# Kernel tuning notes

Hardware: AMD Instinct MI355X
Metric: run time of the kernel (lower is better)

The kernel has to match this reference:

```python
import jax, jax.numpy as jnp
import numpy as np

B, T, S, D, H, DK = 2, 2048, 2048, 1024, 16, 64


def setup_inputs() -> dict:
    key = jax.random.key(0)
    ks = jax.random.split(key, 11)
    s = 1.0 / np.sqrt(D)
    return {
        "query": jax.random.normal(ks[0], (B, T, D), jnp.float32),
        "value": jax.random.normal(ks[1], (B, S, D), jnp.float32),
        "key": jax.random.normal(ks[2], (B, S, D), jnp.float32),
        "Wq": jax.random.normal(ks[3], (D, H, DK), jnp.float32) * s,
        "bq": jnp.zeros((H, DK), jnp.float32),
        "Wk": jax.random.normal(ks[4], (D, H, DK), jnp.float32) * s,
        "bk": jnp.zeros((H, DK), jnp.float32),
        "Wv": jax.random.normal(ks[5], (D, H, DK), jnp.float32) * s,
        "bv": jnp.zeros((H, DK), jnp.float32),
        "Wo": jax.random.normal(ks[6], (H, DK, D), jnp.float32) * (1.0 / np.sqrt(H * DK)),
        "bo": jnp.zeros((D,), jnp.float32),
    }


def reference(query, value, key, Wq, bq, Wk, bk, Wv, bv, Wo, bo):
    # Projections: (B, seq, D) x (D, H, DK) -> (B, seq, H, DK)
    q = jnp.einsum("btd,dhk->bthk", query, Wq) + bq
    k = jnp.einsum("bsd,dhk->bshk", key, Wk) + bk
    v = jnp.einsum("bsd,dhk->bshk", value, Wv) + bv
    # Scaled dot-product attention (keras scales query by 1/sqrt(key_dim))
    q = q * (1.0 / np.sqrt(DK)).astype(np.float32)
    scores = jnp.einsum("bshk,bthk->bhts", k, q)  # (B, H, T, S)
    probs = jax.nn.softmax(scores, axis=-1)
    attn = jnp.einsum("bhts,bshk->bthk", probs, v)  # (B, T, H, DK)
    # Output projection back to model dim
    out = jnp.einsum("bthk,hkd->btd", attn, Wo) + bo
    return out
```

## Files before the change

### kernel.cpp

```cpp
#include <hip/hip_runtime.h>
#include <math.h>

#define BB  2
#define TT  2048
#define SSQ 2048
#define DD  1024
#define HH  16
#define DKK 64
#define MM  (BB*TT)
#define NN  (HH*DKK)

typedef __attribute__((ext_vector_type(8))) short short8;
typedef __attribute__((ext_vector_type(4))) float f32x4;
typedef __attribute__((ext_vector_type(2))) unsigned int u32x2;

__device__ __forceinline__ short f2bf(float x) {
    unsigned u = __builtin_bit_cast(unsigned, x);
    unsigned r = (u + 0x7FFFu + ((u >> 16) & 1u)) >> 16;
    return (short)r;
}

__device__ __forceinline__ void glds16(const void* g, void* l) {
    __builtin_amdgcn_global_load_lds(
        (const __attribute__((address_space(1))) void*)g,
        (__attribute__((address_space(3))) void*)l, 16, 0, 0);
}

__global__ __launch_bounds__(256)
void to_bf16_acts(const float* __restrict__ a0, const float* __restrict__ a1,
                  const float* __restrict__ a2,
                  short* __restrict__ o0, short* __restrict__ o1,
                  short* __restrict__ o2)
{
    int z = blockIdx.y;
    const float* in = (z == 0) ? a0 : (z == 1) ? a1 : a2;
    short* out = (z == 0) ? o0 : (z == 1) ? o1 : o2;
    size_t i0 = ((size_t)blockIdx.x * 256 + threadIdx.x) * 8;
    f32x4 f0 = *(const f32x4*)(in + i0);
    f32x4 f1 = *(const f32x4*)(in + i0 + 4);
    short8 v;
#pragma unroll
    for (int j = 0; j < 4; j++) v[j] = f2bf(f0[j]);
#pragma unroll
    for (int j = 0; j < 4; j++) v[4 + j] = f2bf(f1[j]);
    *(short8*)(out + i0) = v;
}

__global__ __launch_bounds__(256)
void wtrans(const float* __restrict__ w0, const float* __restrict__ w1,
            const float* __restrict__ w2, const float* __restrict__ w3,
            short* __restrict__ t0, short* __restrict__ t1,
            short* __restrict__ t2, short* __restrict__ t3)
{
    __shared__ float Ls[64][65];
    int z = blockIdx.z;
    const float* in = (z == 0) ? w0 : (z == 1) ? w1 : (z == 2) ? w2 : w3;
    short* out = (z == 0) ? t0 : (z == 1) ? t1 : (z == 2) ? t2 : t3;
    const int r0 = blockIdx.y * 64, c0 = blockIdx.x * 64;
    const int t = threadIdx.x;
    const int r = t >> 2, c4 = t & 3;

    const float* src = in + (size_t)(r0 + r) * DD + c0 + c4 * 16;
#pragma unroll
    for (int i = 0; i < 4; i++) {
        f32x4 f = *(const f32x4*)(src + i * 4);
#pragma unroll
        for (int j = 0; j < 4; j++) Ls[r][c4 * 16 + i * 4 + j] = f[j];
    }
    __syncthreads();

    short8 va, vb;
#pragma unroll
    for (int j = 0; j < 8; j++) va[j] = f2bf(Ls[c4 * 16 + j][r]);
#pragma unroll
    for (int j = 0; j < 8; j++) vb[j] = f2bf(Ls[c4 * 16 + 8 + j][r]);
    short* dst = out + (size_t)(c0 + r) * DD + r0 + c4 * 16;
    *(short8*)dst = va;
    *(short8*)(dst + 8) = vb;
}

__global__ __launch_bounds__(256)
void vtrans(const short* __restrict__ in, short* __restrict__ out)
{
    __shared__ short Ls[64][72];
    const int bh = blockIdx.y;
    const int t0 = blockIdx.x * 64;
    const int tid = threadIdx.x;
    const int r = tid >> 2, c4 = tid & 3;

    const short* src = in + ((size_t)bh * TT + t0 + r) * DKK + c4 * 16;
    *(short8*)&Ls[r][c4 * 16]     = *(const short8*)(src);
    *(short8*)&Ls[r][c4 * 16 + 8] = *(const short8*)(src + 8);
    __syncthreads();

    short8 a, b;
#pragma unroll
    for (int j = 0; j < 8; j++) a[j] = Ls[c4 * 16 + j][r];
#pragma unroll
    for (int j = 0; j < 8; j++) b[j] = Ls[c4 * 16 + 8 + j][r];
    short* dst = out + ((size_t)bh * DKK + r) * SSQ + t0 + c4 * 16;
    *(short8*)dst = a;
    *(short8*)(dst + 8) = b;
}

__device__ __forceinline__ void gemm_core(const short* __restrict__ A,
                                          const short* __restrict__ Bt,
                                          int m0, int n0,
                                          short* As, short* Bs,
                                          f32x4 (&acc)[4][4])
{
    const int tid = threadIdx.x;
    const int w = tid >> 6, l = tid & 63;
    const int l15 = l & 15, quad = l >> 4;
    const int wm = w >> 1, wn = w & 1;

#pragma unroll
    for (int i = 0; i < 4; i++)
#pragma unroll
        for (int j = 0; j < 4; j++) acc[i][j] = (f32x4){0.f, 0.f, 0.f, 0.f};

    const int r = tid >> 2, cseg = tid & 3;
    const short* gA = A + (size_t)(m0 + r) * DD + cseg * 8;
    const short* gB = Bt + (size_t)(n0 + r) * DD + cseg * 8;
    short* ldsA = As + w * 512;
    short* ldsB = Bs + w * 512;

    for (int k0 = 0; k0 < DD; k0 += 32) {
        glds16(gA + k0,                 ldsA);
        glds16(gA + (size_t)64 * DD + k0, ldsA + 2048);
        glds16(gB + k0,                 ldsB);
        glds16(gB + (size_t)64 * DD + k0, ldsB + 2048);
        __syncthreads();

        short8 bF[4];
#pragma unroll
        for (int ni = 0; ni < 4; ni++)
            bF[ni] = *(const short8*)&Bs[(wn * 64 + ni * 16 + l15) * 32 + quad * 8];
#pragma unroll
        for (int mi = 0; mi < 4; mi++) {
            short8 aF = *(const short8*)&As[(wm * 64 + mi * 16 + l15) * 32 + quad * 8];
#pragma unroll
            for (int ni = 0; ni < 4; ni++)
                acc[mi][ni] = __builtin_amdgcn_mfma_f32_16x16x32_bf16(aF, bF[ni], acc[mi][ni], 0, 0, 0);
        }
        __syncthreads();
    }
}

__global__ __launch_bounds__(256, 3)
void gemm_qkv(const short* __restrict__ Aq, const short* __restrict__ Ak,
              const short* __restrict__ Av,
              const short* __restrict__ Wqt, const short* __restrict__ Wkt,
              const short* __restrict__ Wvt,
              const float* __restrict__ bq, const float* __restrict__ bk,
              const float* __restrict__ bv,
              short* __restrict__ Qb, short* __restrict__ Kb,
              short* __restrict__ Vtmp)
{
    __shared__ short As[128 * 32];
    __shared__ short Bs[128 * 32];
    const int z = blockIdx.z;
    const short* A  = (z == 0) ? Aq : (z == 1) ? Ak : Av;
    const short* Bt = (z == 0) ? Wqt : (z == 1) ? Wkt : Wvt;
    const float* bias = (z == 0) ? bq : (z == 1) ? bk : bv;
    short* dst = (z == 0) ? Qb : (z == 1) ? Kb : Vtmp;
    const int m0 = blockIdx.y * 128, n0 = blockIdx.x * 128;

    f32x4 acc[4][4];
    gemm_core(A, Bt, m0, n0, As, Bs, acc);

    const int tid = threadIdx.x;
    const int w = tid >> 6, l = tid & 63;
    const int l15 = l & 15, quad = l >> 4;
    const int wm = w >> 1, wn = w & 1;
    const float scale = (z == 0) ? 0.1803368801f : 1.0f;

#pragma unroll
    for (int mi = 0; mi < 4; mi++) {
#pragma unroll
        for (int reg = 0; reg < 4; reg++) {
            int m = m0 + wm * 64 + mi * 16 + quad * 4 + reg;
            int b = m >> 11, t = m & 2047;
#pragma unroll
            for (int ni = 0; ni < 4; ni++) {
                int n = n0 + wn * 64 + ni * 16 + l15;
                float vv = (acc[mi][ni][reg] + bias[n]) * scale;
                int h = n >> 6, dk = n & 63;
                dst[((size_t)(b * HH + h) * TT + t) * DKK + dk] = f2bf(vv);
            }
        }
    }
}

__global__ __launch_bounds__(256, 3)
void gemm_out(const short* __restrict__ Ab, const short* __restrict__ Wot,
              const float* __restrict__ bo, float* __restrict__ out)
{
    __shared__ short As[128 * 32];
    __shared__ short Bs[128 * 32];
    const int m0 = blockIdx.y * 128, n0 = blockIdx.x * 128;

    f32x4 acc[4][4];
    gemm_core(Ab, Wot, m0, n0, As, Bs, acc);

    const int tid = threadIdx.x;
    const int w = tid >> 6, l = tid & 63;
    const int l15 = l & 15, quad = l >> 4;
    const int wm = w >> 1, wn = w & 1;

#pragma unroll
    for (int mi = 0; mi < 4; mi++) {
#pragma unroll
        for (int reg = 0; reg < 4; reg++) {
            int m = m0 + wm * 64 + mi * 16 + quad * 4 + reg;
#pragma unroll
            for (int ni = 0; ni < 4; ni++) {
                int n = n0 + wn * 64 + ni * 16 + l15;
                out[(size_t)m * DD + n] = acc[mi][ni][reg] + bo[n];
            }
        }
    }
}

__global__ __launch_bounds__(256, 2)
void attn_mfma(const short* __restrict__ Qb, const short* __restrict__ Kb,
               const short* __restrict__ Vbt, short* __restrict__ Ab)
{
    __shared__ short QPs[128 * 72];
    __shared__ short Ks[2][64 * 72];
    __shared__ short Vs[2][64 * 72];

    const int tid = threadIdx.x;
    const int w = tid >> 6, l = tid & 63;
    const int l15 = l & 15, quad = l >> 4;
    const int bh = blockIdx.y;
    const int t0 = blockIdx.x * 128;
    const size_t hb = (size_t)bh * SSQ * DKK;
    const int r = tid >> 2, c4 = tid & 3;

    {
        int r2 = tid >> 1, half = tid & 1;
        const short* g = Qb + hb + (size_t)(t0 + r2) * 64 + half * 32;
        short* s = QPs + r2 * 72 + half * 32;
        *(short8*)(s + 0)  = *(const short8*)(g + 0);
        *(short8*)(s + 8)  = *(const short8*)(g + 8);
        *(short8*)(s + 16) = *(const short8*)(g + 16);
        *(short8*)(s + 24) = *(const short8*)(g + 24);
    }
    __threadfence_block();
    short8 qf[2][2];
#pragma unroll
    for (int mf = 0; mf < 2; mf++)
#pragma unroll
        for (int kk = 0; kk < 2; kk++)
            qf[mf][kk] = *(const short8*)&QPs[(32 * w + 16 * mf + l15) * 72 + kk * 32 + quad * 8];

    const short* gkb = Kb + hb + (size_t)r * 64 + c4 * 16;
    const short* gvb = Vbt + hb + (size_t)r * SSQ + c4 * 16;
    short8 kr0 = *(const short8*)(gkb + 0);
    short8 kr1 = *(const short8*)(gkb + 8);
    short8 vr0 = *(const short8*)(gvb + 0);
    short8 vr1 = *(const short8*)(gvb + 8);

    f32x4 o[2][4];
#pragma unroll
    for (int mf = 0; mf < 2; mf++)
#pragma unroll
        for (int j = 0; j < 4; j++) o[mf][j] = (f32x4){0.f, 0.f, 0.f, 0.f};
    float lsum[2] = {0.f, 0.f};

    short* skb = &Ks[0][0] + r * 72 + c4 * 16;
    short* svb = &Vs[0][0] + r * 72 + c4 * 16;

    for (int s0 = 0; s0 < SSQ; s0 += 64) {
        const int bo = (s0 & 64) ? (64 * 72) : 0;
        *(short8*)(skb + bo)     = kr0;
        *(short8*)(skb + bo + 8) = kr1;
        *(short8*)(svb + bo)     = vr0;
        *(short8*)(svb + bo + 8) = vr1;
        if (s0 + 64 < SSQ) {
            const short* gk = gkb + (size_t)(s0 + 64) * 64;
            const short* gv = gvb + (s0 + 64);
            kr0 = *(const short8*)(gk + 0);
            kr1 = *(const short8*)(gk + 8);
            vr0 = *(const short8*)(gv + 0);
            vr1 = *(const short8*)(gv + 8);
        }
        __syncthreads();

        const short* kb_ = &Ks[0][0] + bo;
        const short* vb_ = &Vs[0][0] + bo;

        f32x4 sc[4][2];
#pragma unroll
        for (int np = 0; np < 4; np++)
#pragma unroll
            for (int mf = 0; mf < 2; mf++) sc[np][mf] = (f32x4){0.f, 0.f, 0.f, 0.f};
        __builtin_amdgcn_s_setprio(1);
#pragma unroll
        for (int kk = 0; kk < 2; kk++) {
#pragma unroll
            for (int np = 0; np < 4; np++) {
                short8 aK = *(const short8*)&kb_[(16 * np + l15) * 72 + kk * 32 + quad * 8];
                sc[np][0] = __builtin_amdgcn_mfma_f32_16x16x32_bf16(aK, qf[0][kk], sc[np][0], 0, 0, 0);
                sc[np][1] = __builtin_amdgcn_mfma_f32_16x16x32_bf16(aK, qf[1][kk], sc[np][1], 0, 0, 0);
            }
        }
        __builtin_amdgcn_s_setprio(0);

#pragma unroll
        for (int mf = 0; mf < 2; mf++) {
            short* pr = QPs + (32 * w + 16 * mf + l15) * 72 + 4 * quad;
            float ls = lsum[mf];
#pragma unroll
            for (int np = 0; np < 4; np++) {
                float p0 = __builtin_amdgcn_exp2f(sc[np][mf][0]);
                float p1 = __builtin_amdgcn_exp2f(sc[np][mf][1]);
                float p2 = __builtin_amdgcn_exp2f(sc[np][mf][2]);
                float p3 = __builtin_amdgcn_exp2f(sc[np][mf][3]);
                ls += (p0 + p1) + (p2 + p3);
                unsigned lo = (__builtin_bit_cast(unsigned, p1) & 0xFFFF0000u) |
                              (__builtin_bit_cast(unsigned, p0) >> 16);
                unsigned hi = (__builtin_bit_cast(unsigned, p3) & 0xFFFF0000u) |
                              (__builtin_bit_cast(unsigned, p2) >> 16);
                u32x2 uv;
                uv[0] = lo;
                uv[1] = hi;
                *(u32x2*)(pr + 16 * np) = uv;
            }
            lsum[mf] = ls;
        }
        __threadfence_block();

        __builtin_amdgcn_s_setprio(1);
#pragma unroll
        for (int kk = 0; kk < 2; kk++) {
            short8 aP0 = *(const short8*)&QPs[(32 * w + l15) * 72 + kk * 32 + quad * 8];
            short8 aP1 = *(const short8*)&QPs[(32 * w + 16 + l15) * 72 + kk * 32 + quad * 8];
#pragma unroll
            for (int np = 0; np < 4; np++) {
                short8 bV = *(const short8*)&vb_[(16 * np + l15) * 72 + kk * 32 + quad * 8];
                o[0][np] = __builtin_amdgcn_mfma_f32_16x16x32_bf16(aP0, bV, o[0][np], 0, 0, 0);
                o[1][np] = __builtin_amdgcn_mfma_f32_16x16x32_bf16(aP1, bV, o[1][np], 0, 0, 0);
            }
        }
        __builtin_amdgcn_s_setprio(0);
    }

    const int b = bh >> 4, h = bh & 15;
#pragma unroll
    for (int mf = 0; mf < 2; mf++) {
        float ls = lsum[mf];
        ls += __shfl_xor(ls, 16);
        ls += __shfl_xor(ls, 32);
        float inv = 1.f / ls;
#pragma unroll
        for (int reg = 0; reg < 4; reg++) {
            float invr = __shfl(inv, quad * 4 + reg);
            int t = t0 + 32 * w + 16 * mf + quad * 4 + reg;
#pragma unroll
            for (int np = 0; np < 4; np++) {
                Ab[((size_t)(b * TT + t) * HH + h) * DKK + 16 * np + l15] =
                    f2bf(o[mf][np][reg] * invr);
            }
        }
    }
}

extern "C" void kernel_launch(void* const* d_in, const int* in_sizes, int n_in,
                              void* d_out, int out_size, void* d_ws, size_t ws_size,
                              hipStream_t stream)
{
    const float* query = (const float*)d_in[0];
    const float* value = (const float*)d_in[1];
    const float* key   = (const float*)d_in[2];
    const float* Wq    = (const float*)d_in[3];
    const float* bq    = (const float*)d_in[4];
    const float* Wk    = (const float*)d_in[5];
    const float* bk    = (const float*)d_in[6];
    const float* Wv    = (const float*)d_in[7];
    const float* bv    = (const float*)d_in[8];
    const float* Wo    = (const float*)d_in[9];
    const float* bo    = (const float*)d_in[10];
    float* out = (float*)d_out;

    const size_t actE = (size_t)MM * DD;
    const size_t wE   = (size_t)DD * NN;
    short* p = (short*)d_ws;
    short* Aq   = p; p += actE;
    short* Ak   = p; p += actE;
    short* Av   = p; p += actE;
    short* Wqt  = p; p += wE;
    short* Wkt  = p; p += wE;
    short* Wvt  = p; p += wE;
    short* Wot  = p; p += wE;
    short* Qb   = p; p += actE;
    short* Kb   = p; p += actE;
    short* Vtmp = p; p += actE;
    short* Vbt  = p; p += actE;
    short* Ab   = p; p += actE;

    dim3 blk(256);

    to_bf16_acts<<<dim3((unsigned)(actE / 2048), 3), blk, 0, stream>>>(
        query, key, value, Aq, Ak, Av);

    wtrans<<<dim3(16, 16, 4), blk, 0, stream>>>(Wq, Wk, Wv, Wo, Wqt, Wkt, Wvt, Wot);

    gemm_qkv<<<dim3(NN / 128, MM / 128, 3), blk, 0, stream>>>(
        Aq, Ak, Av, Wqt, Wkt, Wvt, bq, bk, bv, Qb, Kb, Vtmp);

    vtrans<<<dim3(TT / 64, BB * HH), blk, 0, stream>>>(Vtmp, Vbt);

    attn_mfma<<<dim3(TT / 128, BB * HH), blk, 0, stream>>>(Qb, Kb, Vbt, Ab);

    gemm_out<<<dim3(DD / 128, MM / 128), blk, 0, stream>>>(Ab, Wot, bo, out);
}
```

Baseline: 233.4 us.

## Split attention KV range across two wave groups and keep P in registers

The attention kernel now launches 512 threads per block. Two groups of four waves each process half of the key/value sequence and merge their partial outputs and row sums through LDS at the end. Q fragments are loaded straight from global memory, and the probability tile is rearranged into MFMA operand layout with permlane32/16 swaps instead of a round trip through LDS. This doubles the waves per tile and removes the P store/reload, at the cost of a final reduction pass and larger LDS use per block, which may limit how many blocks fit on a CU.

```diff
diff --git a/kernel.cpp b/kernel.cpp
--- a/kernel.cpp
+++ b/kernel.cpp
@@ -12,12 +12,18 @@
 
 typedef __attribute__((ext_vector_type(8))) short short8;
 typedef __attribute__((ext_vector_type(4))) float f32x4;
-typedef __attribute__((ext_vector_type(2))) unsigned int u32x2;
+typedef __attribute__((ext_vector_type(2))) unsigned int uint2v;
+typedef __attribute__((ext_vector_type(4))) unsigned int u32x4;
 
 __device__ __forceinline__ short f2bf(float x) {
     unsigned u = __builtin_bit_cast(unsigned, x);
     unsigned r = (u + 0x7FFFu + ((u >> 16) & 1u)) >> 16;
     return (short)r;
+}
+
+__device__ __forceinline__ unsigned pk2(float lo, float hi) {
+    return (__builtin_bit_cast(unsigned, hi) & 0xFFFF0000u) |
+           (__builtin_bit_cast(unsigned, lo) >> 16);
 }
 
 __device__ __forceinline__ void glds16(const void* g, void* l) {
@@ -222,41 +228,32 @@
     }
 }
 
-__global__ __launch_bounds__(256, 2)
+__global__ __launch_bounds__(512, 4)
 void attn_mfma(const short* __restrict__ Qb, const short* __restrict__ Kb,
                const short* __restrict__ Vbt, short* __restrict__ Ab)
 {
-    __shared__ short QPs[128 * 72];
-    __shared__ short Ks[2][64 * 72];
-    __shared__ short Vs[2][64 * 72];
+    __shared__ short KV[2 * 2 * 2 * 64 * 72];
 
     const int tid = threadIdx.x;
     const int w = tid >> 6, l = tid & 63;
+    const int wq = w & 3, half = w >> 2;
     const int l15 = l & 15, quad = l >> 4;
     const int bh = blockIdx.y;
     const int t0 = blockIdx.x * 128;
     const size_t hb = (size_t)bh * SSQ * DKK;
-    const int r = tid >> 2, c4 = tid & 3;
-
-    {
-        int r2 = tid >> 1, half = tid & 1;
-        const short* g = Qb + hb + (size_t)(t0 + r2) * 64 + half * 32;
-        short* s = QPs + r2 * 72 + half * 32;
-        *(short8*)(s + 0)  = *(const short8*)(g + 0);
-        *(short8*)(s + 8)  = *(const short8*)(g + 8);
-        *(short8*)(s + 16) = *(const short8*)(g + 16);
-        *(short8*)(s + 24) = *(const short8*)(g + 24);
-    }
-    __threadfence_block();
+    const int th = tid & 255;
+    const int r = th >> 2, c4 = th & 3;
+
     short8 qf[2][2];
 #pragma unroll
     for (int mf = 0; mf < 2; mf++)
 #pragma unroll
         for (int kk = 0; kk < 2; kk++)
-            qf[mf][kk] = *(const short8*)&QPs[(32 * w + 16 * mf + l15) * 72 + kk * 32 + quad * 8];
-
-    const short* gkb = Kb + hb + (size_t)r * 64 + c4 * 16;
-    const short* gvb = Vbt + hb + (size_t)r * SSQ + c4 * 16;
+            qf[mf][kk] = *(const short8*)(Qb + hb +
+                (size_t)(t0 + 32 * wq + 16 * mf + l15) * DKK + kk * 32 + quad * 8);
+
+    const short* gkb = Kb + hb + (size_t)(half * 1024 + r) * DKK + c4 * 16;
+    const short* gvb = Vbt + hb + (size_t)r * SSQ + half * 1024 + c4 * 16;
     short8 kr0 = *(const short8*)(gkb + 0);
     short8 kr1 = *(const short8*)(gkb + 8);
     short8 vr0 = *(const short8*)(gvb + 0);
@@ -269,17 +266,17 @@
         for (int j = 0; j < 4; j++) o[mf][j] = (f32x4){0.f, 0.f, 0.f, 0.f};
     float lsum[2] = {0.f, 0.f};
 
-    short* skb = &Ks[0][0] + r * 72 + c4 * 16;
-    short* svb = &Vs[0][0] + r * 72 + c4 * 16;
-
-    for (int s0 = 0; s0 < SSQ; s0 += 64) {
-        const int bo = (s0 & 64) ? (64 * 72) : 0;
-        *(short8*)(skb + bo)     = kr0;
-        *(short8*)(skb + bo + 8) = kr1;
-        *(short8*)(svb + bo)     = vr0;
-        *(short8*)(svb + bo + 8) = vr1;
-        if (s0 + 64 < SSQ) {
-            const short* gk = gkb + (size_t)(s0 + 64) * 64;
+    short* skb = KV + half * 18432 + r * 72 + c4 * 16;
+    const short* khalf0 = KV + half * 18432;
+
+    for (int s0 = 0; s0 < 1024; s0 += 64) {
+        const int dbo = (s0 & 64) ? 9216 : 0;
+        *(short8*)(skb + dbo)          = kr0;
+        *(short8*)(skb + dbo + 8)      = kr1;
+        *(short8*)(skb + dbo + 4608)   = vr0;
+        *(short8*)(skb + dbo + 4616)   = vr1;
+        if (s0 + 64 < 1024) {
+            const short* gk = gkb + (size_t)(s0 + 64) * DKK;
             const short* gv = gvb + (s0 + 64);
             kr0 = *(const short8*)(gk + 0);
             kr1 = *(const short8*)(gk + 8);
@@ -287,9 +284,8 @@
             vr1 = *(const short8*)(gv + 8);
         }
         __syncthreads();
-
-        const short* kb_ = &Ks[0][0] + bo;
-        const short* vb_ = &Vs[0][0] + bo;
+        const short* kb_ = khalf0 + dbo;
+        const short* vb_ = kb_ + 4608;
 
         f32x4 sc[4][2];
 #pragma unroll
@@ -308,60 +304,90 @@
         }
         __builtin_amdgcn_s_setprio(0);
 
+        short8 pa[2][2];
 #pragma unroll
         for (int mf = 0; mf < 2; mf++) {
-            short* pr = QPs + (32 * w + 16 * mf + l15) * 72 + 4 * quad;
+            float pe[4][4];
             float ls = lsum[mf];
 #pragma unroll
             for (int np = 0; np < 4; np++) {
-                float p0 = __builtin_amdgcn_exp2f(sc[np][mf][0]);
-                float p1 = __builtin_amdgcn_exp2f(sc[np][mf][1]);
-                float p2 = __builtin_amdgcn_exp2f(sc[np][mf][2]);
-                float p3 = __builtin_amdgcn_exp2f(sc[np][mf][3]);
-                ls += (p0 + p1) + (p2 + p3);
-                unsigned lo = (__builtin_bit_cast(unsigned, p1) & 0xFFFF0000u) |
-                              (__builtin_bit_cast(unsigned, p0) >> 16);
-                unsigned hi = (__builtin_bit_cast(unsigned, p3) & 0xFFFF0000u) |
-                              (__builtin_bit_cast(unsigned, p2) >> 16);
-                u32x2 uv;
-                uv[0] = lo;
-                uv[1] = hi;
-                *(u32x2*)(pr + 16 * np) = uv;
+#pragma unroll
+                for (int reg = 0; reg < 4; reg++) {
+                    float p = __builtin_amdgcn_exp2f(sc[np][mf][reg]);
+                    pe[np][reg] = p;
+                    ls += p;
+                }
             }
             lsum[mf] = ls;
-        }
-        __threadfence_block();
+#pragma unroll
+            for (int kk = 0; kk < 2; kk++) {
+                u32x4 wd;
+#pragma unroll
+                for (int b = 0; b < 2; b++) {
+                    unsigned Xw = pk2(pe[2 * kk][2 * b],     pe[2 * kk][2 * b + 1]);
+                    unsigned Yw = pk2(pe[2 * kk + 1][2 * b], pe[2 * kk + 1][2 * b + 1]);
+                    uint2v s1 = __builtin_amdgcn_permlane32_swap(Xw, Yw, false, false);
+                    uint2v s2 = __builtin_amdgcn_permlane16_swap(s1[0], s1[1], false, false);
+                    wd[b]     = s2[0];
+                    wd[2 + b] = s2[1];
+                }
+                pa[mf][kk] = __builtin_bit_cast(short8, wd);
+            }
+        }
 
         __builtin_amdgcn_s_setprio(1);
 #pragma unroll
         for (int kk = 0; kk < 2; kk++) {
-            short8 aP0 = *(const short8*)&QPs[(32 * w + l15) * 72 + kk * 32 + quad * 8];
-            short8 aP1 = *(const short8*)&QPs[(32 * w + 16 + l15) * 72 + kk * 32 + quad * 8];
 #pragma unroll
             for (int np = 0; np < 4; np++) {
                 short8 bV = *(const short8*)&vb_[(16 * np + l15) * 72 + kk * 32 + quad * 8];
-                o[0][np] = __builtin_amdgcn_mfma_f32_16x16x32_bf16(aP0, bV, o[0][np], 0, 0, 0);
-                o[1][np] = __builtin_amdgcn_mfma_f32_16x16x32_bf16(aP1, bV, o[1][np], 0, 0, 0);
+                o[0][np] = __builtin_amdgcn_mfma_f32_16x16x32_bf16(pa[0][kk], bV, o[0][np], 0, 0, 0);
+                o[1][np] = __builtin_amdgcn_mfma_f32_16x16x32_bf16(pa[1][kk], bV, o[1][np], 0, 0, 0);
             }
         }
         __builtin_amdgcn_s_setprio(0);
     }
 
-    const int b = bh >> 4, h = bh & 15;
-#pragma unroll
-    for (int mf = 0; mf < 2; mf++) {
-        float ls = lsum[mf];
-        ls += __shfl_xor(ls, 16);
-        ls += __shfl_xor(ls, 32);
-        float inv = 1.f / ls;
-#pragma unroll
-        for (int reg = 0; reg < 4; reg++) {
-            float invr = __shfl(inv, quad * 4 + reg);
-            int t = t0 + 32 * w + 16 * mf + quad * 4 + reg;
+    __syncthreads();
+    float* F = (float*)KV;
+    const int slot = (wq * 64 + l) * 36;
+    if (half == 1) {
+#pragma unroll
+        for (int mf = 0; mf < 2; mf++)
+#pragma unroll
+            for (int np = 0; np < 4; np++)
+                *(f32x4*)&F[slot + (mf * 4 + np) * 4] = o[mf][np];
+        F[slot + 32] = lsum[0];
+        F[slot + 33] = lsum[1];
+    }
+    __syncthreads();
+    if (half == 0) {
+#pragma unroll
+        for (int mf = 0; mf < 2; mf++) {
 #pragma unroll
             for (int np = 0; np < 4; np++) {
-                Ab[((size_t)(b * TT + t) * HH + h) * DKK + 16 * np + l15] =
-                    f2bf(o[mf][np][reg] * invr);
+                f32x4 po = *(const f32x4*)&F[slot + (mf * 4 + np) * 4];
+                o[mf][np] += po;
+            }
+            lsum[mf] += F[slot + 32 + mf];
+        }
+
+        const int b = bh >> 4, h = bh & 15;
+#pragma unroll
+        for (int mf = 0; mf < 2; mf++) {
+            float ls = lsum[mf];
+            ls += __shfl_xor(ls, 16);
+            ls += __shfl_xor(ls, 32);
+            float inv = 1.f / ls;
+#pragma unroll
+            for (int reg = 0; reg < 4; reg++) {
+                float invr = __shfl(inv, quad * 4 + reg);
+                int t = t0 + 32 * wq + 16 * mf + quad * 4 + reg;
+#pragma unroll
+                for (int np = 0; np < 4; np++) {
+                    Ab[((size_t)(b * TT + t) * HH + h) * DKK + 16 * np + l15] =
+                        f2bf(o[mf][np][reg] * invr);
+                }
             }
         }
     }
@@ -412,7 +438,7 @@
 
     vtrans<<<dim3(TT / 64, BB * HH), blk, 0, stream>>>(Vtmp, Vbt);
 
-    attn_mfma<<<dim3(TT / 128, BB * HH), blk, 0, stream>>>(Qb, Kb, Vbt, Ab);
+    attn_mfma<<<dim3(TT / 128, BB * HH), dim3(512), 0, stream>>>(Qb, Kb, Vbt, Ab);
 
     gemm_out<<<dim3(DD / 128, MM / 128), blk, 0, stream>>>(Ab, Wot, bo, out);
 }
```

Result: no change. 235.3 us (+0.8%).
